# Performance work log

Measured on AMD Instinct MI355X. Metric: run time of the kernel, lower is better.

The kernel has to match this reference:

```python
import jax, jax.numpy as jnp
import numpy as np

N = 768      # sentence length n
E = 256      # embedding_dim (== 2*H so layer inputs stack)
H = 128      # lstm_hidden_dim
NL = 2       # lstm_num_layers
F = 128      # fc_hidden_dim


def _run_dir(x, Wih, Whh, b):
    """One LSTM direction over x:(T, in). PyTorch gate order i,f,g,o."""
    pre = x @ Wih.T + b  # (T, 4H), precomputed input contribution
    Hd = Whh.shape[1]
    def step(carry, p):
        h, c = carry
        g = p + Whh @ h
        i, f, gg, o = jnp.split(g, 4)
        i = jax.nn.sigmoid(i)
        f = jax.nn.sigmoid(f)
        gg = jnp.tanh(gg)
        o = jax.nn.sigmoid(o)
        c = f * c + i * gg
        h = o * jnp.tanh(c)
        return (h, c), h
    h0 = jnp.zeros((Hd,), x.dtype)
    _, hs = jax.lax.scan(step, (h0, h0), pre)
    return hs  # (T, H)


def _bilstm(x, Wih, Whh, bih, bhh):
    # Wih: (NL, 2, 4H, in), eval mode (no inter-layer dropout)
    for l in range(Wih.shape[0]):
        hf = _run_dir(x, Wih[l, 0], Whh[l, 0], bih[l, 0] + bhh[l, 0])
        hb = jnp.flip(_run_dir(jnp.flip(x, 0), Wih[l, 1], Whh[l, 1], bih[l, 1] + bhh[l, 1]), 0)
        x = jnp.concatenate([hf, hb], axis=-1)  # (T, 2H)
    return x


def setup_inputs() -> dict:
    key = jax.random.key(0)
    ks = jax.random.split(key, 12)
    s = 0.08
    return {
        "sentence_embedded": jax.random.normal(ks[0], (N, E), jnp.float32),
        "deps": jax.random.randint(ks[1], (N,), 0, N + 1),
        "root_vec": jax.random.uniform(ks[2], (1, E), jnp.float32),
        "Wih": jax.random.normal(ks[3], (NL, 2, 4 * H, E), jnp.float32) * s,
        "Whh": jax.random.normal(ks[4], (NL, 2, 4 * H, H), jnp.float32) * s,
        "bih": jax.random.normal(ks[5], (NL, 2, 4 * H), jnp.float32) * s,
        "bhh": jax.random.normal(ks[6], (NL, 2, 4 * H), jnp.float32) * s,
        "W1": jax.random.normal(ks[7], (F, 4 * H), jnp.float32) * s,
        "b1": jax.random.normal(ks[8], (F,), jnp.float32) * s,
        "w2": jax.random.normal(ks[9], (F,), jnp.float32) * s,
        "b2": jax.random.normal(ks[10], (1,), jnp.float32) * s,
    }


def reference(sentence_embedded, deps, root_vec, Wih, Whh, bih, bhh, W1, b1, w2, b2):
    n = sentence_embedded.shape[0]
    x = jnp.concatenate([sentence_embedded, root_vec], axis=0)  # (n+1, E)
    L = _bilstm(x, Wih, Whh, bih, bhh)                          # (n+1, 2H)
    d = L.shape[1]
    # mlp(concat(L[i], L[j])) computed for all pairs by splitting fc1:
    # fc1(concat(a,b)) = a @ W1a.T + b @ W1b.T + b1
    W1a, W1b = W1[:, :d], W1[:, d:]
    A = L @ W1a.T          # (n+1, F) head-side projection
    B = L[:n] @ W1b.T      # (n, F)   dependent-side projection
    Hact = jnp.tanh(A[:, None, :] + B[None, :, :] + b1)  # (n+1, n, F)
    scores = Hact @ w2 + b2[0]                           # (n+1, n)
    # diagonal (i == j, i < n) set to -inf as in the torch loop
    mask = jnp.arange(n + 1)[:, None] == jnp.arange(n)[None, :]
    return jnp.where(mask, -jnp.inf, scores)
```

## Files before the change

kernel.cpp:

```cpp
#include <hip/hip_runtime.h>
#include <hip/hip_fp8.h>

#define T_SEQ 769
#define N_SENT 768
#define E_IN 256
#define HID 128
#define G4 512
#define F_DIM 128

typedef float f32x4 __attribute__((ext_vector_type(4)));
typedef int i32x8 __attribute__((ext_vector_type(8)));

#if __has_builtin(__builtin_amdgcn_rcpf)
#define RCPF(x) __builtin_amdgcn_rcpf(x)
#else
#define RCPF(x) (1.0f / (x))
#endif

#if __has_builtin(__builtin_amdgcn_exp2f)
#define EXP2F(x) __builtin_amdgcn_exp2f(x)
#else
#define EXP2F(x) __builtin_exp2f(x)
#endif

#define LDS_BARRIER() asm volatile("s_waitcnt lgkmcnt(0)\n\ts_barrier" ::: "memory")

#define L2E 1.4426950408889634f

__device__ __forceinline__ float sigm_fast(float x) {
    return RCPF(1.0f + EXP2F(-L2E * x));
}
__device__ __forceinline__ float tanh_fast(float x) {
    return fmaf(2.0f, RCPF(1.0f + EXP2F(-2.0f * L2E * x)), -1.0f);
}

__device__ __forceinline__ unsigned char f32_to_e4m3(float x) {
#if __has_builtin(__builtin_amdgcn_cvt_pk_fp8_f32)
    return (unsigned char)(__builtin_amdgcn_cvt_pk_fp8_f32(x, x, 0, false) & 0xFF);
#else
    __hip_fp8_e4m3 q(x);
    return (unsigned char)q.__x;
#endif
}

__device__ __forceinline__ int pack4_e4m3(float w0, float w1, float w2, float w3) {
#if __has_builtin(__builtin_amdgcn_cvt_pk_fp8_f32)
    int r = __builtin_amdgcn_cvt_pk_fp8_f32(w0, w1, 0, false);
    return __builtin_amdgcn_cvt_pk_fp8_f32(w2, w3, r, true);
#else
    unsigned x = 0;
    __hip_fp8_e4m3 q0(w0), q1(w1), q2(w2), q3(w3);
    x |= (unsigned)q0.__x;
    x |= (unsigned)q1.__x << 8;
    x |= (unsigned)q2.__x << 16;
    x |= (unsigned)q3.__x << 24;
    return (int)x;
#endif
}

__device__ __forceinline__ float quad_bcast(float x, const int sel) {
#if __has_builtin(__builtin_amdgcn_mov_dpp)
    int ctrl = sel * 0x55;
    int r;
    switch (ctrl) {
        case 0x00: r = __builtin_amdgcn_mov_dpp(__float_as_int(x), 0x00, 0xF, 0xF, true); break;
        case 0x55: r = __builtin_amdgcn_mov_dpp(__float_as_int(x), 0x55, 0xF, 0xF, true); break;
        case 0xAA: r = __builtin_amdgcn_mov_dpp(__float_as_int(x), 0xAA, 0xF, 0xF, true); break;
        default:   r = __builtin_amdgcn_mov_dpp(__float_as_int(x), 0xFF, 0xF, 0xF, true); break;
    }
    return __int_as_float(r);
#else
    int lane = __lane_id();
    return __shfl(x, (lane & ~3) + sel, 64);
#endif
}

__global__ __launch_bounds__(256) void pre_gemm_l0(
    const float* __restrict__ sent, const float* __restrict__ root,
    const float* __restrict__ Wih, const float* __restrict__ bih,
    const float* __restrict__ bhh, float* __restrict__ pre)
{
    const int d = blockIdx.z;
    const float* B = Wih + (size_t)d * G4 * E_IN;
    const float* b0 = bih + (size_t)d * G4;
    const float* b1 = bhh + (size_t)d * G4;
    float* C = pre + (size_t)d * T_SEQ * G4;

    __shared__ __align__(16) float As[16][68];
    __shared__ __align__(16) float Bs[16][68];
    int tid = threadIdx.x;
    int tx = tid & 15, ty = tid >> 4;
    int m0 = blockIdx.x * 64, n0 = blockIdx.y * 64;
    float acc[4][4] = {};
    int lrow = tid >> 2;
    int lk = (tid & 3) << 2;

    for (int k0 = 0; k0 < E_IN; k0 += 16) {
        int m = m0 + lrow;
        float4 av = make_float4(0.f, 0.f, 0.f, 0.f);
        if (m < T_SEQ) {
            int ar = d ? (N_SENT - m) : m;
            av = (ar < N_SENT)
                     ? *(const float4*)(sent + (size_t)ar * E_IN + k0 + lk)
                     : *(const float4*)(root + k0 + lk);
        }
        As[lk + 0][lrow] = av.x; As[lk + 1][lrow] = av.y;
        As[lk + 2][lrow] = av.z; As[lk + 3][lrow] = av.w;
        float4 bv = *(const float4*)(B + (size_t)(n0 + lrow) * E_IN + k0 + lk);
        Bs[lk + 0][lrow] = bv.x; Bs[lk + 1][lrow] = bv.y;
        Bs[lk + 2][lrow] = bv.z; Bs[lk + 3][lrow] = bv.w;
        __syncthreads();
        #pragma unroll
        for (int k = 0; k < 16; ++k) {
            float4 a4 = *(const float4*)&As[k][ty * 4];
            float4 b4 = *(const float4*)&Bs[k][tx * 4];
            float aa[4] = {a4.x, a4.y, a4.z, a4.w};
            float bb[4] = {b4.x, b4.y, b4.z, b4.w};
            #pragma unroll
            for (int i = 0; i < 4; ++i)
                #pragma unroll
                for (int j = 0; j < 4; ++j)
                    acc[i][j] = fmaf(aa[i], bb[j], acc[i][j]);
        }
        __syncthreads();
    }
    float bias[4];
    #pragma unroll
    for (int j = 0; j < 4; ++j) {
        int n = n0 + tx * 4 + j;
        bias[j] = b0[n] + b1[n];
    }
    #pragma unroll
    for (int i = 0; i < 4; ++i) {
        int m = m0 + ty * 4 + i;
        if (m < T_SEQ) {
            #pragma unroll
            for (int j = 0; j < 4; ++j)
                C[(size_t)m * G4 + n0 + tx * 4 + j] = acc[i][j] + bias[j];
        }
    }
}

__global__ __launch_bounds__(256) void pre_gemm_l1(
    const float* __restrict__ L0,
    const float* __restrict__ Wih, const float* __restrict__ bih,
    const float* __restrict__ bhh, float* __restrict__ pre)
{
    const int d = blockIdx.z;
    const float* B = Wih + (size_t)(2 + d) * G4 * E_IN;
    const float* b0 = bih + (size_t)(2 + d) * G4;
    const float* b1 = bhh + (size_t)(2 + d) * G4;
    float* C = pre + (size_t)d * T_SEQ * G4;

    __shared__ __align__(16) float As[16][68];
    __shared__ __align__(16) float Bs[16][68];
    int tid = threadIdx.x;
    int tx = tid & 15, ty = tid >> 4;
    int m0 = blockIdx.x * 64, n0 = blockIdx.y * 64;
    float acc[4][4] = {};
    int lrow = tid >> 2;
    int lk = (tid & 3) << 2;

    for (int k0 = 0; k0 < 256; k0 += 16) {
        int m = m0 + lrow;
        float4 av = make_float4(0.f, 0.f, 0.f, 0.f);
        if (m < T_SEQ) {
            int ar = d ? (N_SENT - m) : m;
            av = *(const float4*)(L0 + (size_t)ar * 256 + k0 + lk);
        }
        As[lk + 0][lrow] = av.x; As[lk + 1][lrow] = av.y;
        As[lk + 2][lrow] = av.z; As[lk + 3][lrow] = av.w;
        float4 bv = *(const float4*)(B + (size_t)(n0 + lrow) * 256 + k0 + lk);
        Bs[lk + 0][lrow] = bv.x; Bs[lk + 1][lrow] = bv.y;
        Bs[lk + 2][lrow] = bv.z; Bs[lk + 3][lrow] = bv.w;
        __syncthreads();
        #pragma unroll
        for (int k = 0; k < 16; ++k) {
            float4 a4 = *(const float4*)&As[k][ty * 4];
            float4 b4 = *(const float4*)&Bs[k][tx * 4];
            float aa[4] = {a4.x, a4.y, a4.z, a4.w};
            float bb[4] = {b4.x, b4.y, b4.z, b4.w};
            #pragma unroll
            for (int i = 0; i < 4; ++i)
                #pragma unroll
                for (int j = 0; j < 4; ++j)
                    acc[i][j] = fmaf(aa[i], bb[j], acc[i][j]);
        }
        __syncthreads();
    }
    float bias[4];
    #pragma unroll
    for (int j = 0; j < 4; ++j) {
        int n = n0 + tx * 4 + j;
        bias[j] = b0[n] + b1[n];
    }
    #pragma unroll
    for (int i = 0; i < 4; ++i) {
        int m = m0 + ty * 4 + i;
        if (m < T_SEQ) {
            #pragma unroll
            for (int j = 0; j < 4; ++j)
                C[(size_t)m * G4 + n0 + tx * 4 + j] = acc[i][j] + bias[j];
        }
    }
}

__global__ __launch_bounds__(256) void ab_gemm(
    const float* __restrict__ L1, const float* __restrict__ W1,
    const float* __restrict__ b1, float* __restrict__ Ap,
    float* __restrict__ Bm)
{
    const int z = blockIdx.z;
    const int M = z ? N_SENT : T_SEQ;
    const float* B = W1 + (z ? 256 : 0);
    float* C = z ? Bm : Ap;

    __shared__ __align__(16) float As[16][68];
    __shared__ __align__(16) float Bs[16][68];
    int tid = threadIdx.x;
    int tx = tid & 15, ty = tid >> 4;
    int m0 = blockIdx.x * 64, n0 = blockIdx.y * 64;
    float acc[4][4] = {};
    int lrow = tid >> 2;
    int lk = (tid & 3) << 2;

    for (int k0 = 0; k0 < 256; k0 += 16) {
        int m = m0 + lrow;
        float4 av = make_float4(0.f, 0.f, 0.f, 0.f);
        if (m < M) av = *(const float4*)(L1 + (size_t)m * 256 + k0 + lk);
        As[lk + 0][lrow] = av.x; As[lk + 1][lrow] = av.y;
        As[lk + 2][lrow] = av.z; As[lk + 3][lrow] = av.w;
        float4 bv = *(const float4*)(B + (size_t)(n0 + lrow) * 512 + k0 + lk);
        Bs[lk + 0][lrow] = bv.x; Bs[lk + 1][lrow] = bv.y;
        Bs[lk + 2][lrow] = bv.z; Bs[lk + 3][lrow] = bv.w;
        __syncthreads();
        #pragma unroll
        for (int k = 0; k < 16; ++k) {
            float4 a4 = *(const float4*)&As[k][ty * 4];
            float4 b4 = *(const float4*)&Bs[k][tx * 4];
            float aa[4] = {a4.x, a4.y, a4.z, a4.w};
            float bb[4] = {b4.x, b4.y, b4.z, b4.w};
            #pragma unroll
            for (int i = 0; i < 4; ++i)
                #pragma unroll
                for (int j = 0; j < 4; ++j)
                    acc[i][j] = fmaf(aa[i], bb[j], acc[i][j]);
        }
        __syncthreads();
    }
    float bias[4];
    #pragma unroll
    for (int j = 0; j < 4; ++j) {
        int n = n0 + tx * 4 + j;
        bias[j] = z ? 0.f : b1[n];
    }
    #pragma unroll
    for (int i = 0; i < 4; ++i) {
        int m = m0 + ty * 4 + i;
        if (m < M) {
            #pragma unroll
            for (int j = 0; j < 4; ++j)
                C[(size_t)m * F_DIM + n0 + tx * 4 + j] = acc[i][j] + bias[j];
        }
    }
}

template <int LSTEP>
__device__ __forceinline__ void lstm_loop(
    const float* __restrict__ pp, int po, float* __restrict__ Lrow,
    const i32x8* __restrict__ Bf, unsigned char (*hb)[HID],
    int g, int q, int u, float Ag, float Bg, float Cg, bool qb0, bool qb1)
{
    float p0 = pp[po];            pp += G4;
    float p1v = pp[po];           pp += G4;
    float p2v = pp[po];           pp += G4;

    f32x4 a0 = {0.f, 0.f, 0.f, 0.f};
    f32x4 a1 = {0.f, 0.f, 0.f, 0.f};
    f32x4 a2 = {0.f, 0.f, 0.f, 0.f};
    f32x4 a3 = {0.f, 0.f, 0.f, 0.f};
    float c = 0.f;
    __syncthreads();

    #pragma unroll 4
    for (int s = 0; s < T_SEQ; ++s) {
        const uint4* hp = (const uint4*)&hb[s & 1][q * 32];
        uint4 lo = hp[0];
        uint4 hi = hp[1];
        i32x8 Af = {(int)lo.x, (int)lo.y, (int)lo.z, (int)lo.w,
                    (int)hi.x, (int)hi.y, (int)hi.z, (int)hi.w};

        float p3 = pp[po];
        pp += G4;

        a0[0] = p0; a1[0] = p0; a2[0] = p0; a3[0] = p0;
        a0 = __builtin_amdgcn_mfma_scale_f32_16x16x128_f8f6f4(
            Af, Bf[0], a0, 0, 0, 0, 0x7F7F7F7F, 0, 0x7F7F7F7F);
        a1 = __builtin_amdgcn_mfma_scale_f32_16x16x128_f8f6f4(
            Af, Bf[1], a1, 0, 0, 0, 0x7F7F7F7F, 0, 0x7F7F7F7F);
        a2 = __builtin_amdgcn_mfma_scale_f32_16x16x128_f8f6f4(
            Af, Bf[2], a2, 0, 0, 0, 0x7F7F7F7F, 0, 0x7F7F7F7F);
        a3 = __builtin_amdgcn_mfma_scale_f32_16x16x128_f8f6f4(
            Af, Bf[3], a3, 0, 0, 0, 0x7F7F7F7F, 0, 0x7F7F7F7F);

        float xa = qb0 ? a1[0] : a0[0];
        float xb = qb0 ? a3[0] : a2[0];
        float x = qb1 ? xb : xa;
        float act = fmaf(Ag, RCPF(1.0f + EXP2F(Bg * x)), Cg);

        float gi = quad_bcast(act, 0);
        float gf = quad_bcast(act, 1);
        float gg = quad_bcast(act, 2);
        float go = quad_bcast(act, 3);

        c = fmaf(gf, c, gi * gg);
        float h = go * tanh_fast(c);
        if (g == 0) {
            hb[(s + 1) & 1][u] = f32_to_e4m3(h);
        }
        LDS_BARRIER();
        if (g == 0) {
            Lrow[0] = h;
        }
        Lrow += LSTEP;
        p0 = p1v; p1v = p2v; p2v = p3;
    }
}

__global__ __launch_bounds__(512)
__attribute__((amdgpu_waves_per_eu(2, 2)))
void lstm_layer(
    const float* __restrict__ pre,
    const float* __restrict__ Whh,
    float* __restrict__ L)
{
    const int d = blockIdx.x;
    const int t = threadIdx.x;
    const int wv = t >> 6;
    const int l = t & 63;
    const int g = l & 3;
    const int v = (l >> 2) & 3;
    const int q = l >> 4;
    const int u = wv * 16 + 4 * q + v;
    const int c15 = l & 15;

    __shared__ __align__(16) unsigned char hb[2][HID];

    i32x8 Bf[4];
    #pragma unroll
    for (int j = 0; j < 4; ++j) {
        int row = (c15 & 3) * HID + wv * 16 + 4 * j + (c15 >> 2);
        const float* wr = Whh + ((size_t)d * G4 + row) * HID + q * 32;
        i32x8 bv;
        #pragma unroll
        for (int w8 = 0; w8 < 8; ++w8) {
            bv[w8] = pack4_e4m3(wr[w8 * 4 + 0], wr[w8 * 4 + 1],
                                wr[w8 * 4 + 2], wr[w8 * 4 + 3]);
        }
        Bf[j] = bv;
    }

    if (t < HID) { hb[0][t] = 0; hb[1][t] = 0; }

    const float Ag = (g == 2) ? 2.0f : 1.0f;
    const float Bg = (g == 2) ? (-2.0f * L2E) : (-L2E);
    const float Cg = (g == 2) ? -1.0f : 0.0f;
    const bool qb0 = (q & 1) != 0;
    const bool qb1 = (q & 2) != 0;

    const float* pp = pre + (size_t)d * T_SEQ * G4;
    const int po = g * HID + u;
    float* Lrow = L + (size_t)(d ? N_SENT : 0) * 256 + d * HID + u;

    if (d == 0) {
        lstm_loop<256>(pp, po, Lrow, Bf, hb, g, q, u, Ag, Bg, Cg, qb0, qb1);
    } else {
        lstm_loop<-256>(pp, po, Lrow, Bf, hb, g, q, u, Ag, Bg, Cg, qb0, qb1);
    }
}

__global__ __launch_bounds__(256) void scores_k(
    const float* __restrict__ Ap,
    const float* __restrict__ Bm,
    const float* __restrict__ w2,
    const float* __restrict__ b2,
    float* __restrict__ out)
{
    __shared__ __align__(16) float Asl[32][132];
    __shared__ __align__(16) float Bsl[32][132];
    __shared__ __align__(16) float w2s[F_DIM];
    int tid = threadIdx.x;
    int i0 = blockIdx.x * 32, j0 = blockIdx.y * 32;

    for (int e = tid; e < 1024; e += 256) {
        int r = e >> 5;
        int qq = (e & 31) << 2;
        float4 av = (i0 + r < T_SEQ)
                        ? *(const float4*)(Ap + (size_t)(i0 + r) * F_DIM + qq)
                        : make_float4(0.f, 0.f, 0.f, 0.f);
        *(float4*)&Asl[r][qq] = av;
        float4 bv = *(const float4*)(Bm + (size_t)(j0 + r) * F_DIM + qq);
        *(float4*)&Bsl[r][qq] = bv;
    }
    if (tid < 32) {
        *(float4*)&w2s[tid * 4] = *(const float4*)(w2 + tid * 4);
    }
    __syncthreads();

    int tx = tid & 15, ty = tid >> 4;
    float s[2][2] = {};
    #pragma unroll 8
    for (int k4 = 0; k4 < F_DIM; k4 += 4) {
        float4 a0 = *(const float4*)&Asl[ty * 2][k4];
        float4 a1 = *(const float4*)&Asl[ty * 2 + 1][k4];
        float4 b0 = *(const float4*)&Bsl[tx * 2][k4];
        float4 b1v = *(const float4*)&Bsl[tx * 2 + 1][k4];
        float4 wv = *(const float4*)&w2s[k4];
        float aa[2][4] = {{a0.x, a0.y, a0.z, a0.w}, {a1.x, a1.y, a1.z, a1.w}};
        float bb[2][4] = {{b0.x, b0.y, b0.z, b0.w}, {b1v.x, b1v.y, b1v.z, b1v.w}};
        float ww[4] = {wv.x, wv.y, wv.z, wv.w};
        #pragma unroll
        for (int kk = 0; kk < 4; ++kk)
            #pragma unroll
            for (int ii = 0; ii < 2; ++ii)
                #pragma unroll
                for (int jj = 0; jj < 2; ++jj)
                    s[ii][jj] = fmaf(ww[kk],
                                     tanh_fast(aa[ii][kk] + bb[jj][kk]),
                                     s[ii][jj]);
    }

    float bb2 = b2[0];
    #pragma unroll
    for (int ii = 0; ii < 2; ++ii) {
        int i = i0 + ty * 2 + ii;
        if (i < T_SEQ) {
            #pragma unroll
            for (int jj = 0; jj < 2; ++jj) {
                int j = j0 + tx * 2 + jj;
                out[(size_t)i * N_SENT + j] =
                    (i == j) ? -1.0e30f : (s[ii][jj] + bb2);
            }
        }
    }
}

extern "C" void kernel_launch(void* const* d_in, const int* in_sizes, int n_in,
                              void* d_out, int out_size, void* d_ws, size_t ws_size,
                              hipStream_t stream) {
    const float* sent = (const float*)d_in[0];
    const float* root = (const float*)d_in[2];
    const float* Wih  = (const float*)d_in[3];
    const float* Whh  = (const float*)d_in[4];
    const float* bih  = (const float*)d_in[5];
    const float* bhh  = (const float*)d_in[6];
    const float* W1   = (const float*)d_in[7];
    const float* b1   = (const float*)d_in[8];
    const float* w2   = (const float*)d_in[9];
    const float* b2   = (const float*)d_in[10];
    float* out = (float*)d_out;
    float* ws = (float*)d_ws;

    float* pre = ws;
    float* L0  = pre + 2 * T_SEQ * G4;
    float* L1  = L0 + T_SEQ * 256;
    float* Ap  = L1 + T_SEQ * 256;
    float* Bm  = Ap + T_SEQ * F_DIM;

    dim3 b256(256);

    pre_gemm_l0<<<dim3(13, 8, 2), b256, 0, stream>>>(sent, root, Wih, bih, bhh, pre);
    lstm_layer<<<2, 512, 0, stream>>>(pre, Whh, L0);

    pre_gemm_l1<<<dim3(13, 8, 2), b256, 0, stream>>>(L0, Wih, bih, bhh, pre);
    lstm_layer<<<2, 512, 0, stream>>>(pre, Whh + (size_t)2 * G4 * HID, L1);

    ab_gemm<<<dim3(13, 2, 2), b256, 0, stream>>>(L1, W1, b1, Ap, Bm);

    scores_k<<<dim3(25, 24), b256, 0, stream>>>(Ap, Bm, w2, b2, out);
}
```

Baseline: 782.9 us.

## Run both LSTM directions in one 1024-thread block sharing a CU

```diff
diff --git a/kernel.cpp b/kernel.cpp
--- a/kernel.cpp
+++ b/kernel.cpp
@@ -27,9 +27,6 @@
 
 #define L2E 1.4426950408889634f
 
-__device__ __forceinline__ float sigm_fast(float x) {
-    return RCPF(1.0f + EXP2F(-L2E * x));
-}
 __device__ __forceinline__ float tanh_fast(float x) {
     return fmaf(2.0f, RCPF(1.0f + EXP2F(-2.0f * L2E * x)), -1.0f);
 }
@@ -265,15 +262,59 @@
     }
 }
 
-template <int LSTEP>
-__device__ __forceinline__ void lstm_loop(
-    const float* __restrict__ pp, int po, float* __restrict__ Lrow,
-    const i32x8* __restrict__ Bf, unsigned char (*hb)[HID],
-    int g, int q, int u, float Ag, float Bg, float Cg, bool qb0, bool qb1)
+__global__ __launch_bounds__(1024)
+__attribute__((amdgpu_waves_per_eu(4, 4)))
+void lstm_layer(
+    const float* __restrict__ pre,
+    const float* __restrict__ Whh,
+    float* __restrict__ L)
 {
+    const int t = threadIdx.x;
+    const int dg = t >> 9;
+    const int tid = t & 511;
+    const int wv = tid >> 6;
+    const int l = tid & 63;
+    const int g = l & 3;
+    const int v = (l >> 2) & 3;
+    const int q = l >> 4;
+    const int u = wv * 16 + 4 * q + v;
+    const int c15 = l & 15;
+
+    __shared__ __align__(16) unsigned char hb[2][2][HID];
+
+    i32x8 Bf[4];
+    #pragma unroll
+    for (int j = 0; j < 4; ++j) {
+        int row = (c15 & 3) * HID + wv * 16 + 4 * j + (c15 >> 2);
+        const float* wr = Whh + ((size_t)dg * G4 + row) * HID + q * 32;
+        i32x8 bv;
+        #pragma unroll
+        for (int w8 = 0; w8 < 8; ++w8) {
+            bv[w8] = pack4_e4m3(wr[w8 * 4 + 0], wr[w8 * 4 + 1],
+                                wr[w8 * 4 + 2], wr[w8 * 4 + 3]);
+        }
+        Bf[j] = bv;
+    }
+
+    if (t < 2 * HID) {
+        hb[t >> 7][0][t & 127] = 0;
+        hb[t >> 7][1][t & 127] = 0;
+    }
+
+    const float Ag = (g == 2) ? 2.0f : 1.0f;
+    const float Bg = (g == 2) ? (-2.0f * L2E) : (-L2E);
+    const float Cg = (g == 2) ? -1.0f : 0.0f;
+    const bool qb0 = (q & 1) != 0;
+    const bool qb1 = (q & 2) != 0;
+
+    const float* pp = pre + (size_t)dg * T_SEQ * G4;
+    const int po = g * HID + u;
     float p0 = pp[po];            pp += G4;
     float p1v = pp[po];           pp += G4;
     float p2v = pp[po];           pp += G4;
+
+    float* Lrow = L + (size_t)(dg ? N_SENT : 0) * 256 + dg * HID + u;
+    const ptrdiff_t ldelta = dg ? -(ptrdiff_t)256 : (ptrdiff_t)256;
 
     f32x4 a0 = {0.f, 0.f, 0.f, 0.f};
     f32x4 a1 = {0.f, 0.f, 0.f, 0.f};
@@ -284,7 +325,7 @@
 
     #pragma unroll 4
     for (int s = 0; s < T_SEQ; ++s) {
-        const uint4* hp = (const uint4*)&hb[s & 1][q * 32];
+        const uint4* hp = (const uint4*)&hb[dg][s & 1][q * 32];
         uint4 lo = hp[0];
         uint4 hi = hp[1];
         i32x8 Af = {(int)lo.x, (int)lo.y, (int)lo.z, (int)lo.w,
@@ -314,68 +355,16 @@
         float go = quad_bcast(act, 3);
 
         c = fmaf(gf, c, gi * gg);
-        float h = go * tanh_fast(c);
-        if (g == 0) {
-            hb[(s + 1) & 1][u] = f32_to_e4m3(h);
-        }
-        LDS_BARRIER();
+        float R = RCPF(1.0f + EXP2F(-2.0f * L2E * c));
+        float go2 = go + go;
+        float h = fmaf(go2, R, -go);
         if (g == 0) {
             Lrow[0] = h;
-        }
-        Lrow += LSTEP;
+            hb[dg][(s + 1) & 1][u] = f32_to_e4m3(h);
+        }
+        Lrow += ldelta;
         p0 = p1v; p1v = p2v; p2v = p3;
-    }
-}
-
-__global__ __launch_bounds__(512)
-__attribute__((amdgpu_waves_per_eu(2, 2)))
-void lstm_layer(
-    const float* __restrict__ pre,
-    const float* __restrict__ Whh,
-    float* __restrict__ L)
-{
-    const int d = blockIdx.x;
-    const int t = threadIdx.x;
-    const int wv = t >> 6;
-    const int l = t & 63;
-    const int g = l & 3;
-    const int v = (l >> 2) & 3;
-    const int q = l >> 4;
-    const int u = wv * 16 + 4 * q + v;
-    const int c15 = l & 15;
-
-    __shared__ __align__(16) unsigned char hb[2][HID];
-
-    i32x8 Bf[4];
-    #pragma unroll
-    for (int j = 0; j < 4; ++j) {
-        int row = (c15 & 3) * HID + wv * 16 + 4 * j + (c15 >> 2);
-        const float* wr = Whh + ((size_t)d * G4 + row) * HID + q * 32;
-        i32x8 bv;
-        #pragma unroll
-        for (int w8 = 0; w8 < 8; ++w8) {
-            bv[w8] = pack4_e4m3(wr[w8 * 4 + 0], wr[w8 * 4 + 1],
-                                wr[w8 * 4 + 2], wr[w8 * 4 + 3]);
-        }
-        Bf[j] = bv;
-    }
-
-    if (t < HID) { hb[0][t] = 0; hb[1][t] = 0; }
-
-    const float Ag = (g == 2) ? 2.0f : 1.0f;
-    const float Bg = (g == 2) ? (-2.0f * L2E) : (-L2E);
-    const float Cg = (g == 2) ? -1.0f : 0.0f;
-    const bool qb0 = (q & 1) != 0;
-    const bool qb1 = (q & 2) != 0;
-
-    const float* pp = pre + (size_t)d * T_SEQ * G4;
-    const int po = g * HID + u;
-    float* Lrow = L + (size_t)(d ? N_SENT : 0) * 256 + d * HID + u;
-
-    if (d == 0) {
-        lstm_loop<256>(pp, po, Lrow, Bf, hb, g, q, u, Ag, Bg, Cg, qb0, qb1);
-    } else {
-        lstm_loop<-256>(pp, po, Lrow, Bf, hb, g, q, u, Ag, Bg, Cg, qb0, qb1);
+        LDS_BARRIER();
     }
 }
 
@@ -470,10 +459,10 @@
     dim3 b256(256);
 
     pre_gemm_l0<<<dim3(13, 8, 2), b256, 0, stream>>>(sent, root, Wih, bih, bhh, pre);
-    lstm_layer<<<2, 512, 0, stream>>>(pre, Whh, L0);
+    lstm_layer<<<1, 1024, 0, stream>>>(pre, Whh, L0);
 
     pre_gemm_l1<<<dim3(13, 8, 2), b256, 0, stream>>>(L0, Wih, bih, bhh, pre);
-    lstm_layer<<<2, 512, 0, stream>>>(pre, Whh + (size_t)2 * G4 * HID, L1);
+    lstm_layer<<<1, 1024, 0, stream>>>(pre, Whh + (size_t)2 * G4 * HID, L1);
 
     ab_gemm<<<dim3(13, 2, 2), b256, 0, stream>>>(L1, W1, b1, Ap, Bm);
 
```

Result: slower. 886.5 us (+13.2%).
